# Kernel optimization log

Hardware: AMD Instinct MI355X
Metric: run time of the kernel (lower is better)

Reference implementation:

```python
import jax, jax.numpy as jnp
import numpy as np

B = 256      # n_batch
N = 256      # n_x
RHO = 1.0    # control['rho']
N_ITERS = 50 # control['max_iters'], run fixed (no early stop) for determinism


def setup_inputs() -> dict:
    key = jax.random.key(0)
    k1, k2 = jax.random.split(key)
    # Build a well-conditioned symmetric PSD Q (QP requires Q PSD)
    Araw = jax.random.normal(k1, (B, N, N), dtype=jnp.float32)
    Q = jnp.einsum('bij,bkj->bik', Araw, Araw) / N + jnp.eye(N, dtype=jnp.float32)
    p = jax.random.normal(k2, (B, N, 1), dtype=jnp.float32)
    lb = -jnp.ones((B, N, 1), dtype=jnp.float32)
    ub = jnp.ones((B, N, 1), dtype=jnp.float32)
    return {"Q": Q, "p": p, "lb": lb, "ub": ub}


def reference(Q, p, lb, ub):
    n = Q.shape[1]
    # M = Q + rho*I, LU-factored once (rho fixed: adaptive_rho=False)
    M = Q + RHO * jnp.eye(n, dtype=Q.dtype)
    lu, piv = jax.vmap(jax.scipy.linalg.lu_factor)(M)
    solve = jax.vmap(lambda l, pv, r: jax.scipy.linalg.lu_solve((l, pv), r))

    x0 = jnp.zeros_like(p)
    z0 = jnp.zeros_like(p)
    u0 = jnp.zeros_like(p)

    def step(carry, _):
        x, z, u = carry
        rhs = -p + RHO * (z - u)            # [B,N,1]
        x = solve(lu, piv, rhs)             # batched LU solve
        z = jnp.clip(x + u, lb, ub)         # box projection (max with lb, min with ub)
        u = u + (x - z)                     # dual update
        return (x, z, u), None

    (x, z, u), _ = jax.lax.scan(step, (x0, z0, u0), None, length=N_ITERS)
    # scale=False => D=1, so sol x = D*x = x (unroll=True path returns x)
    return x
```

## Files before the change

kernel.cpp:

```cpp
#include <hip/hip_runtime.h>


#define NX     256
#define NITER  50
#define TRIF   33280
#define NTILE  2080
#define NTHR   1024

__device__ __forceinline__ int rowoff(int r) {
    int M = r >> 2, s = r & 3;
    return 4 * (M + 1) * ((M << 1) + s);
}

__launch_bounds__(NTHR, 1)
__global__ void boxqp_blk_kernel(const float* __restrict__ Q,
                                 const float* __restrict__ p,
                                 const float* __restrict__ lb,
                                 const float* __restrict__ ub,
                                 float* __restrict__ out)
{
    extern __shared__ char smem_raw[];
    float*  tri  = (float*)smem_raw;
    float4* tri4 = (float4*)tri;
    float4* P4   = (float4*)(tri + TRIF);
    float4* W4   = P4 + NX;
    float*  vbuf = (float*)(W4 + NX);
    unsigned char* lut = (unsigned char*)(vbuf + 272);

    const int t = threadIdx.x;
    const int b = blockIdx.x;
    const size_t qbase = ((size_t)b) << 16;

    if (t < 64) {
        int base = (t * (t + 1)) >> 1;
        for (int c = 0; c <= t; ++c) lut[base + c] = (unsigned char)t;
    }
    __syncthreads();

    for (int tile = t; tile < NTILE; tile += NTHR) {
        int rb = lut[tile];
        int cb = tile - ((rb * (rb + 1)) >> 1);
        int r0 = rb << 2, j0 = cb << 2;
        int q0 = ((rb + 1) * (rb << 1)) + cb, step = rb + 1;
        if (rb != cb) {
            #pragma unroll
            for (int s2 = 0; s2 < 4; ++s2) {
                float4 v = *(const float4*)(Q + qbase + (size_t)(r0 + s2) * NX + j0);
                tri4[q0 + s2 * step] = v;
            }
        } else {
            #pragma unroll
            for (int s2 = 0; s2 < 4; ++s2) {
                int rr = r0 + s2;
                float4 v = *(const float4*)(Q + qbase + (size_t)rr * NX + j0);
                float4 tq;
                tq.x = (j0 + 0 > rr) ? 0.f : (v.x + ((j0 + 0 == rr) ? 1.f : 0.f));
                tq.y = (j0 + 1 > rr) ? 0.f : (v.y + ((j0 + 1 == rr) ? 1.f : 0.f));
                tq.z = (j0 + 2 > rr) ? 0.f : (v.z + ((j0 + 2 == rr) ? 1.f : 0.f));
                tq.w = (j0 + 3 > rr) ? 0.f : (v.w + ((j0 + 3 == rr) ? 1.f : 0.f));
                tri4[q0 + s2 * step] = tq;
            }
        }
    }
    __syncthreads();

    for (int kb = 0; kb < 64; ++kb) {
        const int k0 = kb << 2;

        if (t < NX) {
            int i = t;
            float4 pv;
            if (i >= k0 + 4) {
                pv = tri4[(rowoff(i) >> 2) + kb];
            } else {
                float v0, v1, v2, v3;
                #pragma unroll
                for (int m = 0; m < 4; ++m) {
                    int km = k0 + m;
                    float vv = (km <= i) ? tri[rowoff(i) + km] : tri[rowoff(km) + i];
                    if (m == 0) v0 = vv; else if (m == 1) v1 = vv;
                    else if (m == 2) v2 = vv; else v3 = vv;
                }
                pv = make_float4(v0, v1, v2, v3);
            }
            P4[i] = pv;
        }
        __syncthreads();

        float S[4][4];
        {
            #pragma unroll
            for (int m = 0; m < 4; ++m) {
                float4 pr = P4[k0 + m];
                S[m][0] = pr.x; S[m][1] = pr.y; S[m][2] = pr.z; S[m][3] = pr.w;
            }
            #pragma unroll
            for (int kk = 0; kk < 4; ++kk) {
                float inv = 1.0f / S[kk][kk];
                #pragma unroll
                for (int a2 = 0; a2 < 4; ++a2) {
                    if (a2 == kk) continue;
                    #pragma unroll
                    for (int b2 = 0; b2 < 4; ++b2) {
                        if (b2 == kk) continue;
                        S[a2][b2] -= S[a2][kk] * S[kk][b2] * inv;
                    }
                }
                #pragma unroll
                for (int a2 = 0; a2 < 4; ++a2) {
                    if (a2 == kk) continue;
                    S[a2][kk] *= inv;
                    S[kk][a2] *= inv;
                }
                S[kk][kk] = -inv;
            }
        }
        if (t < NX) {
            float4 pr = P4[t];
            float4 w;
            w.x = -(pr.x * S[0][0] + pr.y * S[1][0] + pr.z * S[2][0] + pr.w * S[3][0]);
            w.y = -(pr.x * S[0][1] + pr.y * S[1][1] + pr.z * S[2][1] + pr.w * S[3][1]);
            w.z = -(pr.x * S[0][2] + pr.y * S[1][2] + pr.z * S[2][2] + pr.w * S[3][2]);
            w.w = -(pr.x * S[0][3] + pr.y * S[1][3] + pr.z * S[2][3] + pr.w * S[3][3]);
            W4[t] = w;
        }
        __syncthreads();

        for (int tile = t; tile < NTILE; tile += NTHR) {
            int rb = lut[tile];
            int cb = tile - ((rb * (rb + 1)) >> 1);
            int r0 = rb << 2;
            int q0 = ((rb + 1) * (rb << 1)) + cb, step = rb + 1;
            if (rb == kb) {
                if (cb == kb) {
                    #pragma unroll
                    for (int s2 = 0; s2 < 4; ++s2)
                        tri4[q0 + s2 * step] = make_float4(S[s2][0], S[s2][1], S[s2][2], S[s2][3]);
                } else {
                    int j0 = cb << 2;
                    #pragma unroll
                    for (int s2 = 0; s2 < 4; ++s2) {
                        float4 v;
                        v.x = ((const float*)(W4 + j0 + 0))[s2];
                        v.y = ((const float*)(W4 + j0 + 1))[s2];
                        v.z = ((const float*)(W4 + j0 + 2))[s2];
                        v.w = ((const float*)(W4 + j0 + 3))[s2];
                        tri4[q0 + s2 * step] = v;
                    }
                }
            } else if (cb == kb) {
                #pragma unroll
                for (int s2 = 0; s2 < 4; ++s2)
                    tri4[q0 + s2 * step] = W4[r0 + s2];
            } else {
                int j0 = cb << 2;
                float4 Pc0 = P4[j0 + 0], Pc1 = P4[j0 + 1], Pc2 = P4[j0 + 2], Pc3 = P4[j0 + 3];
                #pragma unroll
                for (int s2 = 0; s2 < 4; ++s2) {
                    float4 wr = W4[r0 + s2];
                    float4 tq = tri4[q0 + s2 * step];
                    tq.x -= wr.x * Pc0.x + wr.y * Pc0.y + wr.z * Pc0.z + wr.w * Pc0.w;
                    tq.y -= wr.x * Pc1.x + wr.y * Pc1.y + wr.z * Pc1.z + wr.w * Pc1.w;
                    tq.z -= wr.x * Pc2.x + wr.y * Pc2.y + wr.z * Pc2.z + wr.w * Pc2.w;
                    tq.w -= wr.x * Pc3.x + wr.y * Pc3.y + wr.z * Pc3.z + wr.w * Pc3.w;
                    tri4[q0 + s2 * step] = tq;
                }
            }
        }
        __syncthreads();
    }

    const int r  = t >> 2;
    const int q4 = t & 3;
    const int jc = q4 << 6;
    float mr[64];
    {
        const int offr = rowoff(r);
        #pragma unroll
        for (int jj = 0; jj < 64; ++jj) {
            int j = jc + jj;
            int addr = (j <= r) ? (offr + j) : (rowoff(j) + r);
            mr[jj] = tri[addr];
        }
    }

    const int gb = (b << 8) + r;
    const float pi = p[gb], lbi = lb[gb], ubi = ub[gb];
    const int vw = r + ((r >> 6) << 2);

    float x = 0.f, z = 0.f, u = 0.f;
    __syncthreads();
    for (int it = 0; it < NITER; ++it) {
        if (q4 == 0) vbuf[vw] = (u + pi) - z;
        __syncthreads();
        const float4* vb4 = (const float4*)(vbuf + q4 * 68);
        float a0 = 0.f, a1 = 0.f, a2 = 0.f, a3 = 0.f;
        #pragma unroll
        for (int m = 0; m < 16; ++m) {
            float4 v = vb4[m];
            a0 += mr[4 * m + 0] * v.x;
            a1 += mr[4 * m + 1] * v.y;
            a2 += mr[4 * m + 2] * v.z;
            a3 += mr[4 * m + 3] * v.w;
        }
        float s = (a0 + a1) + (a2 + a3);
        s += __shfl_xor(s, 1);
        s += __shfl_xor(s, 2);
        x = s;
        float xu = x + u;
        z = fminf(fmaxf(xu, lbi), ubi);
        u = xu - z;
        __syncthreads();
    }

    if (q4 == 0) out[gb] = x;
}

extern "C" void kernel_launch(void* const* d_in, const int* in_sizes, int n_in,
                              void* d_out, int out_size, void* d_ws, size_t ws_size,
                              hipStream_t stream) {
    const float* Q  = (const float*)d_in[0];
    const float* p  = (const float*)d_in[1];
    const float* lb = (const float*)d_in[2];
    const float* ub = (const float*)d_in[3];
    float* out = (float*)d_out;

    const size_t shmem = (size_t)TRIF * 4 + NX * 16 + NX * 16 + 272 * 4 + NTILE;
    (void)hipFuncSetAttribute((const void*)boxqp_blk_kernel,
                              hipFuncAttributeMaxDynamicSharedMemorySize,
                              (int)shmem);

    hipLaunchKernelGGL(boxqp_blk_kernel, dim3(256), dim3(NTHR), shmem, stream,
                       Q, p, lb, ub, out);
}
```

Before: 362.0 us.

## Switch in-LDS block inversion to 8-wide panels with register-tiled updates

The Gauss-Jordan style in-place inversion of Q+I moves from 4x4 to 8x8 pivot blocks, which halves the number of panel steps and barriers (32 instead of 64). Each thread now owns one persistent 8x8 tile, so the rank-8 update keeps its accumulators in registers. The 8x8 pivot inversion is done with wave shuffles across 64 lanes, and the panel buffers use an XOR swizzle to avoid LDS bank conflicts. The trade-off is more registers per thread and only 528 of 1024 threads active during updates, plus a serial shuffle chain for the pivot block.

```diff
diff --git a/kernel.cpp b/kernel.cpp
--- a/kernel.cpp
+++ b/kernel.cpp
@@ -4,189 +4,236 @@
 #define NX     256
 #define NITER  50
 #define TRIF   33280
-#define NTILE  2080
 #define NTHR   1024
+#define NREG   528
+#define PTF    264
+
+#define OFF_PT  33280
+#define OFF_WT  35392
+#define OFF_W8  37504
+#define OFF_SL  39552
+#define OFF_VB  39632
+#define LDS_F   39904
 
 __device__ __forceinline__ int rowoff(int r) {
     int M = r >> 2, s = r & 3;
     return 4 * (M + 1) * ((M << 1) + s);
 }
-
-__launch_bounds__(NTHR, 1)
-__global__ void boxqp_blk_kernel(const float* __restrict__ Q,
-                                 const float* __restrict__ p,
-                                 const float* __restrict__ lb,
-                                 const float* __restrict__ ub,
-                                 float* __restrict__ out)
+__device__ __forceinline__ int physq(int q) { return q ^ ((q >> 3) & 7); }
+__device__ __forceinline__ int physf(int i) { return 4 * physq(i >> 2) + (i & 3); }
+
+__launch_bounds__(NTHR, 4)
+__global__ void boxqp_r8_kernel(const float* __restrict__ Q,
+                                const float* __restrict__ p,
+                                const float* __restrict__ lb,
+                                const float* __restrict__ ub,
+                                float* __restrict__ out)
 {
-    extern __shared__ char smem_raw[];
-    float*  tri  = (float*)smem_raw;
+    extern __shared__ float lds[];
+    float*  tri  = lds;
     float4* tri4 = (float4*)tri;
-    float4* P4   = (float4*)(tri + TRIF);
-    float4* W4   = P4 + NX;
-    float*  vbuf = (float*)(W4 + NX);
-    unsigned char* lut = (unsigned char*)(vbuf + 272);
+    float*  PT   = lds + OFF_PT;
+    float*  WT   = lds + OFF_WT;
+    float*  W8   = lds + OFF_W8;
+    float*  SL   = lds + OFF_SL;
+    float*  vbuf = lds + OFF_VB;
 
     const int t = threadIdx.x;
     const int b = blockIdx.x;
     const size_t qbase = ((size_t)b) << 16;
 
-    if (t < 64) {
-        int base = (t * (t + 1)) >> 1;
-        for (int c = 0; c <= t; ++c) lut[base + c] = (unsigned char)t;
+    int rb2, cb2;
+    {
+        int tt = (t < NREG) ? t : 0;
+        int r_ = (int)((sqrtf((float)(8 * tt + 1)) - 1.0f) * 0.5f);
+        while ((r_ + 1) * (r_ + 2) / 2 <= tt) ++r_;
+        while (r_ * (r_ + 1) / 2 > tt) --r_;
+        rb2 = r_;
+        cb2 = tt - ((r_ * (r_ + 1)) >> 1);
+    }
+    const int  r0   = rb2 << 3;
+    const int  j0q  = cb2 << 1;
+    const bool diag = (rb2 == cb2);
+    int rowQ[8];
+    #pragma unroll
+    for (int s2 = 0; s2 < 8; ++s2) rowQ[s2] = rowoff(r0 + s2) >> 2;
+    const int pq0 = physq(j0q), pq1 = physq(j0q + 1);
+
+    if (t < NREG) {
+        #pragma unroll
+        for (int s2 = 0; s2 < 8; ++s2) {
+            const int r = r0 + s2;
+            #pragma unroll
+            for (int h = 0; h < 2; ++h) {
+                if (diag && h == 1 && s2 < 4) continue;
+                const int gq = j0q + h;
+                float4 v = *(const float4*)(Q + qbase + ((size_t)r << 8) + (gq << 2));
+                if (diag) {
+                    const int c0 = gq << 2;
+                    v.x = (c0 + 0 > r) ? 0.f : (v.x + (c0 + 0 == r ? 1.f : 0.f));
+                    v.y = (c0 + 1 > r) ? 0.f : (v.y + (c0 + 1 == r ? 1.f : 0.f));
+                    v.z = (c0 + 2 > r) ? 0.f : (v.z + (c0 + 2 == r ? 1.f : 0.f));
+                    v.w = (c0 + 3 > r) ? 0.f : (v.w + (c0 + 3 == r ? 1.f : 0.f));
+                }
+                tri4[rowQ[s2] + gq] = v;
+            }
+        }
     }
     __syncthreads();
 
-    for (int tile = t; tile < NTILE; tile += NTHR) {
-        int rb = lut[tile];
-        int cb = tile - ((rb * (rb + 1)) >> 1);
-        int r0 = rb << 2, j0 = cb << 2;
-        int q0 = ((rb + 1) * (rb << 1)) + cb, step = rb + 1;
-        if (rb != cb) {
-            #pragma unroll
-            for (int s2 = 0; s2 < 4; ++s2) {
-                float4 v = *(const float4*)(Q + qbase + (size_t)(r0 + s2) * NX + j0);
-                tri4[q0 + s2 * step] = v;
-            }
-        } else {
-            #pragma unroll
-            for (int s2 = 0; s2 < 4; ++s2) {
-                int rr = r0 + s2;
-                float4 v = *(const float4*)(Q + qbase + (size_t)rr * NX + j0);
-                float4 tq;
-                tq.x = (j0 + 0 > rr) ? 0.f : (v.x + ((j0 + 0 == rr) ? 1.f : 0.f));
-                tq.y = (j0 + 1 > rr) ? 0.f : (v.y + ((j0 + 1 == rr) ? 1.f : 0.f));
-                tq.z = (j0 + 2 > rr) ? 0.f : (v.z + ((j0 + 2 == rr) ? 1.f : 0.f));
-                tq.w = (j0 + 3 > rr) ? 0.f : (v.w + ((j0 + 3 == rr) ? 1.f : 0.f));
-                tri4[q0 + s2 * step] = tq;
-            }
-        }
-    }
-    __syncthreads();
-
-    for (int kb = 0; kb < 64; ++kb) {
-        const int k0 = kb << 2;
-
-        if (t < NX) {
-            int i = t;
-            float4 pv;
-            if (i >= k0 + 4) {
-                pv = tri4[(rowoff(i) >> 2) + kb];
+    const int i1     = t >> 1;
+    const int h1     = t & 1;
+    const int rowQi1 = (i1 < NX) ? (rowoff(i1) >> 2) : 0;
+    const int pfi1   = physf(i1 & 255);
+    const int pfT    = physf(t & 255);
+
+    for (int kb = 0; kb < 32; ++kb) {
+        const int k0 = kb << 3;
+
+        if (t < 512) {
+            const int i = i1;
+            float v0, v1, v2, v3;
+            if (i >= k0 + 8) {
+                float4 v = tri4[rowQi1 + (kb << 1) + h1];
+                v0 = v.x; v1 = v.y; v2 = v.z; v3 = v.w;
             } else {
-                float v0, v1, v2, v3;
-                #pragma unroll
-                for (int m = 0; m < 4; ++m) {
-                    int km = k0 + m;
-                    float vv = (km <= i) ? tri[rowoff(i) + km] : tri[rowoff(km) + i];
-                    if (m == 0) v0 = vv; else if (m == 1) v1 = vv;
-                    else if (m == 2) v2 = vv; else v3 = vv;
-                }
-                pv = make_float4(v0, v1, v2, v3);
-            }
-            P4[i] = pv;
-        }
-        __syncthreads();
-
-        float S[4][4];
-        {
-            #pragma unroll
-            for (int m = 0; m < 4; ++m) {
-                float4 pr = P4[k0 + m];
-                S[m][0] = pr.x; S[m][1] = pr.y; S[m][2] = pr.z; S[m][3] = pr.w;
-            }
-            #pragma unroll
-            for (int kk = 0; kk < 4; ++kk) {
-                float inv = 1.0f / S[kk][kk];
-                #pragma unroll
-                for (int a2 = 0; a2 < 4; ++a2) {
-                    if (a2 == kk) continue;
+                const int roi = rowoff(i);
+                {   int km = k0 + (h1 << 2) + 0;
+                    v0 = (km <= i) ? tri[roi + km] : tri[rowoff(km) + i]; }
+                {   int km = k0 + (h1 << 2) + 1;
+                    v1 = (km <= i) ? tri[roi + km] : tri[rowoff(km) + i]; }
+                {   int km = k0 + (h1 << 2) + 2;
+                    v2 = (km <= i) ? tri[roi + km] : tri[rowoff(km) + i]; }
+                {   int km = k0 + (h1 << 2) + 3;
+                    v3 = (km <= i) ? tri[roi + km] : tri[rowoff(km) + i]; }
+            }
+            const int rbase = (h1 << 2) * PTF + pfi1;
+            PT[rbase + 0 * PTF] = v0;
+            PT[rbase + 1 * PTF] = v1;
+            PT[rbase + 2 * PTF] = v2;
+            PT[rbase + 3 * PTF] = v3;
+        }
+        __syncthreads();
+
+        if (t < 64) {
+            const int a = t >> 3, bb = t & 7;
+            float S = PT[bb * PTF + physf(k0 + a)];
+            #pragma unroll
+            for (int kk = 0; kk < 8; ++kk) {
+                const float dkk = __shfl(S, kk * 9);
+                const float inv = 1.0f / dkk;
+                const float cs  = __shfl(S, (t & 56) | kk);
+                const float rs  = __shfl(S, (kk << 3) | bb);
+                const float upd = S - cs * rs * inv;
+                const bool ad = (a == kk), bd = (bb == kk);
+                S = (ad && bd) ? -inv : (ad ? rs * inv : (bd ? cs * inv : upd));
+            }
+            SL[a * 9 + bb] = S;
+        }
+        __syncthreads();
+
+        if (t < 256) {
+            float pv[8];
+            #pragma unroll
+            for (int m = 0; m < 8; ++m) pv[m] = PT[m * PTF + pfT];
+            float w[8];
+            #pragma unroll
+            for (int c = 0; c < 8; ++c) {
+                float acc = 0.f;
+                #pragma unroll
+                for (int m = 0; m < 8; ++m) acc += pv[m] * SL[m * 9 + c];
+                w[c] = -acc;
+                WT[c * PTF + t] = -acc;
+            }
+            *(float4*)(W8 + (t << 3))     = make_float4(w[0], w[1], w[2], w[3]);
+            *(float4*)(W8 + (t << 3) + 4) = make_float4(w[4], w[5], w[6], w[7]);
+        }
+        __syncthreads();
+
+        if (t < NREG) {
+            if (rb2 == kb) {
+                if (cb2 == kb) {
                     #pragma unroll
-                    for (int b2 = 0; b2 < 4; ++b2) {
-                        if (b2 == kk) continue;
-                        S[a2][b2] -= S[a2][kk] * S[kk][b2] * inv;
+                    for (int s2 = 0; s2 < 8; ++s2) {
+                        #pragma unroll
+                        for (int h = 0; h < 2; ++h) {
+                            if (h == 1 && s2 < 4) continue;
+                            const int c4 = (h << 2);
+                            float4 v = make_float4(SL[s2 * 9 + c4 + 0], SL[s2 * 9 + c4 + 1],
+                                                   SL[s2 * 9 + c4 + 2], SL[s2 * 9 + c4 + 3]);
+                            tri4[rowQ[s2] + j0q + h] = v;
+                        }
                     }
-                }
-                #pragma unroll
-                for (int a2 = 0; a2 < 4; ++a2) {
-                    if (a2 == kk) continue;
-                    S[a2][kk] *= inv;
-                    S[kk][a2] *= inv;
-                }
-                S[kk][kk] = -inv;
-            }
-        }
-        if (t < NX) {
-            float4 pr = P4[t];
-            float4 w;
-            w.x = -(pr.x * S[0][0] + pr.y * S[1][0] + pr.z * S[2][0] + pr.w * S[3][0]);
-            w.y = -(pr.x * S[0][1] + pr.y * S[1][1] + pr.z * S[2][1] + pr.w * S[3][1]);
-            w.z = -(pr.x * S[0][2] + pr.y * S[1][2] + pr.z * S[2][2] + pr.w * S[3][2]);
-            w.w = -(pr.x * S[0][3] + pr.y * S[1][3] + pr.z * S[2][3] + pr.w * S[3][3]);
-            W4[t] = w;
-        }
-        __syncthreads();
-
-        for (int tile = t; tile < NTILE; tile += NTHR) {
-            int rb = lut[tile];
-            int cb = tile - ((rb * (rb + 1)) >> 1);
-            int r0 = rb << 2;
-            int q0 = ((rb + 1) * (rb << 1)) + cb, step = rb + 1;
-            if (rb == kb) {
-                if (cb == kb) {
+                } else {
                     #pragma unroll
-                    for (int s2 = 0; s2 < 4; ++s2)
-                        tri4[q0 + s2 * step] = make_float4(S[s2][0], S[s2][1], S[s2][2], S[s2][3]);
-                } else {
-                    int j0 = cb << 2;
+                    for (int s2 = 0; s2 < 8; ++s2) {
+                        float4 wv0 = *(const float4*)(WT + s2 * PTF + (j0q << 2));
+                        float4 wv1 = *(const float4*)(WT + s2 * PTF + (j0q << 2) + 4);
+                        tri4[rowQ[s2] + j0q + 0] = wv0;
+                        tri4[rowQ[s2] + j0q + 1] = wv1;
+                    }
+                }
+            } else if (cb2 == kb) {
+                #pragma unroll
+                for (int s2 = 0; s2 < 8; ++s2) {
+                    const int r = r0 + s2;
+                    tri4[rowQ[s2] + j0q + 0] = *(const float4*)(W8 + (r << 3));
+                    tri4[rowQ[s2] + j0q + 1] = *(const float4*)(W8 + (r << 3) + 4);
+                }
+            } else {
+                float4 acc[8][2];
+                #pragma unroll
+                for (int s2 = 0; s2 < 8; ++s2) {
+                    acc[s2][0] = tri4[rowQ[s2] + j0q + 0];
+                    acc[s2][1] = tri4[rowQ[s2] + j0q + 1];
+                }
+                #pragma unroll
+                for (int m = 0; m < 8; ++m) {
+                    const float4 pa = *(const float4*)(PT + m * PTF + (pq0 << 2));
+                    const float4 pb = *(const float4*)(PT + m * PTF + (pq1 << 2));
+                    const float4 wa = *(const float4*)(WT + m * PTF + (rb2 << 3));
+                    const float4 wb = *(const float4*)(WT + m * PTF + (rb2 << 3) + 4);
+                    const float ws[8] = {wa.x, wa.y, wa.z, wa.w, wb.x, wb.y, wb.z, wb.w};
                     #pragma unroll
-                    for (int s2 = 0; s2 < 4; ++s2) {
-                        float4 v;
-                        v.x = ((const float*)(W4 + j0 + 0))[s2];
-                        v.y = ((const float*)(W4 + j0 + 1))[s2];
-                        v.z = ((const float*)(W4 + j0 + 2))[s2];
-                        v.w = ((const float*)(W4 + j0 + 3))[s2];
-                        tri4[q0 + s2 * step] = v;
+                    for (int s2 = 0; s2 < 8; ++s2) {
+                        acc[s2][0].x -= ws[s2] * pa.x;
+                        acc[s2][0].y -= ws[s2] * pa.y;
+                        acc[s2][0].z -= ws[s2] * pa.z;
+                        acc[s2][0].w -= ws[s2] * pa.w;
+                        acc[s2][1].x -= ws[s2] * pb.x;
+                        acc[s2][1].y -= ws[s2] * pb.y;
+                        acc[s2][1].z -= ws[s2] * pb.z;
+                        acc[s2][1].w -= ws[s2] * pb.w;
                     }
                 }
-            } else if (cb == kb) {
-                #pragma unroll
-                for (int s2 = 0; s2 < 4; ++s2)
-                    tri4[q0 + s2 * step] = W4[r0 + s2];
-            } else {
-                int j0 = cb << 2;
-                float4 Pc0 = P4[j0 + 0], Pc1 = P4[j0 + 1], Pc2 = P4[j0 + 2], Pc3 = P4[j0 + 3];
-                #pragma unroll
-                for (int s2 = 0; s2 < 4; ++s2) {
-                    float4 wr = W4[r0 + s2];
-                    float4 tq = tri4[q0 + s2 * step];
-                    tq.x -= wr.x * Pc0.x + wr.y * Pc0.y + wr.z * Pc0.z + wr.w * Pc0.w;
-                    tq.y -= wr.x * Pc1.x + wr.y * Pc1.y + wr.z * Pc1.z + wr.w * Pc1.w;
-                    tq.z -= wr.x * Pc2.x + wr.y * Pc2.y + wr.z * Pc2.z + wr.w * Pc2.w;
-                    tq.w -= wr.x * Pc3.x + wr.y * Pc3.y + wr.z * Pc3.z + wr.w * Pc3.w;
-                    tri4[q0 + s2 * step] = tq;
-                }
-            }
-        }
-        __syncthreads();
-    }
-
-    const int r  = t >> 2;
-    const int q4 = t & 3;
+                #pragma unroll
+                for (int s2 = 0; s2 < 8; ++s2) {
+                    tri4[rowQ[s2] + j0q + 0] = acc[s2][0];
+                    if (!(diag && s2 < 4)) tri4[rowQ[s2] + j0q + 1] = acc[s2][1];
+                }
+            }
+        }
+        __syncthreads();
+    }
+
+    const int rr = t >> 2, q4 = t & 3;
     const int jc = q4 << 6;
     float mr[64];
     {
-        const int offr = rowoff(r);
+        const int offr = rowoff(rr);
         #pragma unroll
         for (int jj = 0; jj < 64; ++jj) {
-            int j = jc + jj;
-            int addr = (j <= r) ? (offr + j) : (rowoff(j) + r);
+            const int j = jc + jj;
+            const int addr = (j <= rr) ? (offr + j) : (rowoff(j) + rr);
             mr[jj] = tri[addr];
         }
     }
-
-    const int gb = (b << 8) + r;
+    #pragma unroll
+    for (int jj = 0; jj < 64; ++jj) asm volatile("" : "+v"(mr[jj]));
+
+    const int gb = (b << 8) + rr;
     const float pi = p[gb], lbi = lb[gb], ubi = ub[gb];
-    const int vw = r + ((r >> 6) << 2);
+    const int vw = rr + ((rr >> 6) << 2);
 
     float x = 0.f, z = 0.f, u = 0.f;
     __syncthreads();
@@ -197,7 +244,7 @@
         float a0 = 0.f, a1 = 0.f, a2 = 0.f, a3 = 0.f;
         #pragma unroll
         for (int m = 0; m < 16; ++m) {
-            float4 v = vb4[m];
+            const float4 v = vb4[m];
             a0 += mr[4 * m + 0] * v.x;
             a1 += mr[4 * m + 1] * v.y;
             a2 += mr[4 * m + 2] * v.z;
@@ -207,7 +254,7 @@
         s += __shfl_xor(s, 1);
         s += __shfl_xor(s, 2);
         x = s;
-        float xu = x + u;
+        const float xu = x + u;
         z = fminf(fmaxf(xu, lbi), ubi);
         u = xu - z;
         __syncthreads();
@@ -225,11 +272,11 @@
     const float* ub = (const float*)d_in[3];
     float* out = (float*)d_out;
 
-    const size_t shmem = (size_t)TRIF * 4 + NX * 16 + NX * 16 + 272 * 4 + NTILE;
-    (void)hipFuncSetAttribute((const void*)boxqp_blk_kernel,
+    const size_t shmem = (size_t)LDS_F * 4;
+    (void)hipFuncSetAttribute((const void*)boxqp_r8_kernel,
                               hipFuncAttributeMaxDynamicSharedMemorySize,
                               (int)shmem);
 
-    hipLaunchKernelGGL(boxqp_blk_kernel, dim3(256), dim3(NTHR), shmem, stream,
+    hipLaunchKernelGGL(boxqp_r8_kernel, dim3(256), dim3(NTHR), shmem, stream,
                        Q, p, lb, ub, out);
 }
```

Measured after the change: 789.8 us. 118% more time.
